# Performance work log

Measured on AMD Instinct MI355X. Metric: run time of the kernel, lower is better.

Reference implementation:

```python
import jax, jax.numpy as jnp
import numpy as np
from jax.ops import segment_sum

N = 50000        # nodes
E = 800000       # edges (avg degree 16)
H = 128          # hidden_dim
N_ITER = 2       # BCRefinement n_iterations
TIE_P = 0.05     # fraction of tie (boundary) edges


def setup_inputs() -> dict:
    key = jax.random.key(0)
    ks = jax.random.split(key, 24)
    s = 0.02
    inp = {
        'h': jax.random.normal(ks[0], (N, H), jnp.float32),
        'e': jax.random.normal(ks[1], (E, H), jnp.float32),
        'edge_attr_raw': jax.random.normal(ks[2], (E, 10), jnp.float32),
        # edge_refine: Linear(3H,2H) -> ReLU -> Linear(2H,H)
        'W_er1': s * jax.random.normal(ks[3], (3 * H, 2 * H), jnp.float32),
        'b_er1': jnp.zeros((2 * H,), jnp.float32),
        'W_er2': s * jax.random.normal(ks[4], (2 * H, H), jnp.float32),
        'b_er2': jnp.zeros((H,), jnp.float32),
        # GRUCell(H,H) torch layout: [3H, H] chunks (r, z, n)
        'W_ih': s * jax.random.normal(ks[5], (3 * H, H), jnp.float32),
        'W_hh': s * jax.random.normal(ks[6], (3 * H, H), jnp.float32),
        'b_ih': jnp.zeros((3 * H,), jnp.float32),
        'b_hh': jnp.zeros((3 * H,), jnp.float32),
        # node_neigh_fc: Linear(H,H)
        'W_nn': s * jax.random.normal(ks[7], (H, H), jnp.float32),
        'b_nn': jnp.zeros((H,), jnp.float32),
        # gate_mlp: Linear(3H,H) -> ReLU -> Linear(H,1), last bias init -2.0
        'W_g1': s * jax.random.normal(ks[8], (3 * H, H), jnp.float32),
        'b_g1': jnp.zeros((H,), jnp.float32),
        'W_g2': s * jax.random.normal(ks[9], (H, 1), jnp.float32),
        'b_g2': jnp.full((1,), -2.0, jnp.float32),
        'edge_index': jax.random.randint(ks[10], (2, E), 0, N, jnp.int32),
        'is_tie': jax.random.uniform(ks[11], (E,)) < TIE_P,
    }
    return inp


def reference(h, e, edge_attr_raw,
              W_er1, b_er1, W_er2, b_er2,
              W_ih, W_hh, b_ih, b_hh,
              W_nn, b_nn,
              W_g1, b_g1, W_g2, b_g2,
              edge_index, is_tie):
    row = edge_index[0]
    col = edge_index[1]
    tie_f = is_tie.astype(h.dtype)                        # [E]
    internal = ~is_tie

    # coupling buses: endpoints of any tie edge (tie-incidence count > 0)
    cpl_cnt = segment_sum(tie_f, row, num_segments=N) + \
              segment_sum(tie_f, col, num_segments=N)     # [N]
    is_cpl = cpl_cnt > 0

    # internal edges pointing into coupling buses; b_smooth weights w = 1/sqrt(X^2+eps)
    to_cpl = internal & is_cpl[col]
    X = jnp.abs(edge_attr_raw[:, 1])
    w = jnp.where(to_cpl, 1.0 / jnp.sqrt(X * X + 1e-6), 0.0)
    w_den = segment_sum(w, col, num_segments=N)           # [N]
    w_norm = w / (w_den[col] + 1e-6)                      # [E], zero off-mask

    deg = jnp.maximum(cpl_cnt, 1.0)                       # clamp_min(1.0)

    h_work, e_work = h, e
    for _ in range(N_ITER):
        # --- tie-edge refinement (applied only on tie edges) ---
        edge_in = jnp.concatenate([e_work, h_work[row], h_work[col]], axis=-1)  # [E,3H]
        e_ref = jax.nn.relu(edge_in @ W_er1 + b_er1) @ W_er2 + b_er2            # [E,H]
        e_work = e_work + tie_f[:, None] * e_ref

        # --- node messages from internal neighbors into coupling buses ---
        m_node_msg = h_work[row] @ W_nn + b_nn                                   # [E,H]
        m_node_all = segment_sum(m_node_msg * w_norm[:, None], col,
                                 num_segments=N)                                 # [N,H]

        # --- mean of incident tie-edge features at each node ---
        tie_e = tie_f[:, None] * e_work                                          # [E,H]
        m_edge_all = (segment_sum(tie_e, row, num_segments=N) +
                      segment_sum(tie_e, col, num_segments=N)) / deg[:, None]    # [N,H]

        # --- gating + GRU update on coupling buses ---
        gate_in = jnp.concatenate([m_edge_all, m_node_all, h_work], axis=-1)     # [N,3H]
        gate = jax.nn.sigmoid(jax.nn.relu(gate_in @ W_g1 + b_g1) @ W_g2 + b_g2)  # [N,1]
        m = m_edge_all + gate * m_node_all                                       # [N,H]

        gi = m @ W_ih.T + b_ih                                                   # [N,3H]
        gh = h_work @ W_hh.T + b_hh
        r = jax.nn.sigmoid(gi[:, :H] + gh[:, :H])
        z = jax.nn.sigmoid(gi[:, H:2 * H] + gh[:, H:2 * H])
        n = jnp.tanh(gi[:, 2 * H:] + r * gh[:, 2 * H:])
        h_new = (1.0 - z) * n + z * h_work

        h_work = jnp.where(is_cpl[:, None], h_new, h_work)
    return h_work, e_work
```

## Files before the change

kernel.cpp:

```cpp
#include <hip/hip_runtime.h>
#include <cstdint>

#define N_NODES 50000
#define N_EDGES 800000
#define HDIM    128
#define TIE_CAP 44000
#define NITER   2
#define SCAN_B  256

typedef __attribute__((ext_vector_type(8))) short bf16x8;
typedef __attribute__((ext_vector_type(4))) float f32x4;

__device__ __forceinline__ uint32_t f2bf(float f) {
    uint32_t u = __builtin_bit_cast(uint32_t, f);
    return (u + 0x7fffu + ((u >> 16) & 1u)) >> 16;
}
__device__ __forceinline__ float bf2f(uint32_t b) {
    return __builtin_bit_cast(float, b << 16);
}
__device__ __forceinline__ uint32_t comb2(uint32_t me, uint32_t mn, float g) {
    float a0 = bf2f(me & 0xffffu) + g * bf2f(mn & 0xffffu);
    float a1 = bf2f(me >> 16)     + g * bf2f(mn >> 16);
    return f2bf(a0) | (f2bf(a1) << 16);
}


__device__ __forceinline__ void stage_a128(const float* __restrict__ base,
                                           const int* __restrict__ gidx,
                                           int m0, int Mlim, char* tile, int tid)
{
    const int c = tid & 15;
    #pragma unroll
    for (int p = 0; p < 4; ++p) {
        int row = p * 32 + (tid >> 4);
        int ar = m0 + row; if (ar >= Mlim) ar = Mlim - 1;
        long g = gidx ? gidx[ar] : ar;
        const float* s = base + g * HDIM + c * 4;
        float4 v0 = *(const float4*)s;
        float4 v1 = *(const float4*)(s + 64);
        uint2 w0 = make_uint2(f2bf(v0.x) | (f2bf(v0.y) << 16),
                              f2bf(v0.z) | (f2bf(v0.w) << 16));
        uint2 w1 = make_uint2(f2bf(v1.x) | (f2bf(v1.y) << 16),
                              f2bf(v1.z) | (f2bf(v1.w) << 16));
        int sw = (row & 7) << 4;
        *(uint2*)(tile + row * 256 + ((c * 8) ^ sw)) = w0;
        *(uint2*)(tile + row * 256 + ((c * 8 + 128) ^ sw)) = w1;
    }
}

__device__ __forceinline__ void stage_bf128(const uint16_t* __restrict__ base,
                                            const int* __restrict__ gidx,
                                            int m0, int Mlim, char* tile, int tid)
{
    const int c = tid & 15;
    #pragma unroll
    for (int p = 0; p < 4; ++p) {
        int row = p * 32 + (tid >> 4);
        int ar = m0 + row; if (ar >= Mlim) ar = Mlim - 1;
        long g = gidx ? gidx[ar] : ar;
        uint4 v = *(const uint4*)(base + g * HDIM + c * 8);
        *(uint4*)(tile + row * 256 + ((c * 16) ^ ((row & 7) << 4))) = v;
    }
}

__device__ __forceinline__ void stage_b128(const short* __restrict__ BT, int ldk,
                                           int n0, int k0, char* tile, int tid)
{
    const int c = tid & 15;
    #pragma unroll
    for (int p = 0; p < 4; ++p) {
        int n = p * 32 + (tid >> 4);
        uint4 v = *(const uint4*)&BT[(size_t)(n0 + n) * ldk + k0 + c * 8];
        *(uint4*)(tile + n * 256 + ((c * 16) ^ ((n & 7) << 4))) = v;
    }
}

__device__ __forceinline__ void mfma128(const char* At, const char* Bt,
                                        int wr, int wc, int lane, f32x4 acc[4][2])
{
    #pragma unroll
    for (int ks = 0; ks < 4; ++ks) {
        int kb = ks * 64 + (lane >> 4) * 16;
        bf16x8 aF[4], bF[2];
        #pragma unroll
        for (int mi = 0; mi < 4; ++mi) {
            int row = wr * 64 + mi * 16 + (lane & 15);
            aF[mi] = *(const bf16x8*)(At + row * 256 + (kb ^ ((row & 7) << 4)));
        }
        #pragma unroll
        for (int ni = 0; ni < 2; ++ni) {
            int n = wc * 32 + ni * 16 + (lane & 15);
            bF[ni] = *(const bf16x8*)(Bt + n * 256 + (kb ^ ((n & 7) << 4)));
        }
        #pragma unroll
        for (int mi = 0; mi < 4; ++mi)
            #pragma unroll
            for (int ni = 0; ni < 2; ++ni)
                acc[mi][ni] = __builtin_amdgcn_mfma_f32_16x16x32_bf16(
                    aF[mi], bF[ni], acc[mi][ni], 0, 0, 0);
    }
}

__global__ __launch_bounds__(512)
void k_tie_fused(float* __restrict__ out_e, const uint16_t* __restrict__ h_bf,
                 const int* __restrict__ tie_cnt_p,
                 const int* __restrict__ tie_list, const int* __restrict__ tie_row,
                 const int* __restrict__ tie_col,
                 const short* __restrict__ BTer1, const short* __restrict__ BTer2,
                 const float* __restrict__ b_er1, const float* __restrict__ b_er2,
                 const float* __restrict__ deg_inv, float* __restrict__ m_edge)
{
    int cnt = *tie_cnt_p; if (cnt > TIE_CAP) cnt = TIE_CAP;
    const int m0 = blockIdx.x * 128;
    if (m0 >= cnt) return;

    __shared__ __align__(16) char At[32 * 1024];
    __shared__ __align__(16) char B0[32 * 1024];
    __shared__ __align__(16) char B1[32 * 1024];

    const int tid = threadIdx.x, lane = tid & 63;
    const int wid = tid >> 6, wr = wid >> 2, wc = wid & 3;

    f32x4 acc0[4][2] = {}, acc1[4][2] = {};
    #pragma unroll 1
    for (int c = 0; c < 3; ++c) {
        if (c == 0) stage_a128(out_e, tie_list, m0, cnt, At, tid);
        else        stage_bf128(h_bf, (c == 1) ? tie_row : tie_col, m0, cnt, At, tid);
        stage_b128(BTer1, 384, 0,   c * 128, B0, tid);
        stage_b128(BTer1, 384, 128, c * 128, B1, tid);
        __syncthreads();
        mfma128(At, B0, wr, wc, lane, acc0);
        mfma128(At, B1, wr, wc, lane, acc1);
        __syncthreads();
    }

    #pragma unroll
    for (int half = 0; half < 2; ++half) {
        char* Ct = half ? B0 : At;
        #pragma unroll
        for (int ni = 0; ni < 2; ++ni) {
            int col = wc * 32 + ni * 16 + (lane & 15);
            float bv = b_er1[half * 128 + col];
            #pragma unroll
            for (int mi = 0; mi < 4; ++mi)
                #pragma unroll
                for (int j = 0; j < 4; ++j) {
                    int rl = wr * 64 + mi * 16 + ((lane >> 4) << 2) + j;
                    float v = fmaxf((half ? acc1 : acc0)[mi][ni][j] + bv, 0.f);
                    *(uint16_t*)(Ct + rl * 256 + ((col * 2) ^ ((rl & 7) << 4))) =
                        (uint16_t)f2bf(v);
                }
        }
    }
    stage_b128(BTer2, 256, 0, 0, B1, tid);
    __syncthreads();
    f32x4 acc2[4][2] = {};
    mfma128(At, B1, wr, wc, lane, acc2);
    __syncthreads();
    stage_b128(BTer2, 256, 0, 128, B1, tid);
    __syncthreads();
    mfma128(B0, B1, wr, wc, lane, acc2);

    int col0 = wc * 32 + (lane & 15);
    float bv0 = b_er2[col0], bv1 = b_er2[col0 + 16];
    #pragma unroll
    for (int mi = 0; mi < 4; ++mi) {
        #pragma unroll
        for (int j = 0; j < 4; ++j) {
            int i = m0 + wr * 64 + mi * 16 + ((lane >> 4) << 2) + j;
            if (i < cnt) {
                int e = tie_list[i], r = tie_row[i], cc = tie_col[i];
                float dr = deg_inv[r], dc = deg_inv[cc];
                #pragma unroll
                for (int ni = 0; ni < 2; ++ni) {
                    int col = col0 + ni * 16;
                    float er = acc2[mi][ni][j] + (ni ? bv1 : bv0);
                    size_t eb = (size_t)e * HDIM + col;
                    float v = out_e[eb] + er;
                    out_e[eb] = v;
                    atomicAdd(&m_edge[(size_t)r * HDIM + col], v * dr);
                    atomicAdd(&m_edge[(size_t)cc * HDIM + col], v * dc);
                }
            }
        }
    }
}

__global__ __launch_bounds__(512)
void k_node_mega(const float* __restrict__ m_edge, const uint16_t* __restrict__ agg,
                 float* __restrict__ out_h, uint16_t* __restrict__ h_bf,
                 const float* __restrict__ cpl_cnt, const float* __restrict__ sumw,
                 const short* __restrict__ BTnn, const float* __restrict__ b_nn,
                 const short* __restrict__ BTg1, const float* __restrict__ b_g1,
                 const float* __restrict__ Wg2, const float* __restrict__ b_g2,
                 const short* __restrict__ BTcomb,
                 const short* __restrict__ BTihn, const short* __restrict__ BThhn,
                 const float* __restrict__ b_ih, const float* __restrict__ b_hh)
{
    const int m0 = blockIdx.x * 128;
    __shared__ __align__(16) char Tme[32 * 1024];
    __shared__ __align__(16) char Tmn[32 * 1024];
    __shared__ __align__(16) char Th [32 * 1024];
    __shared__ __align__(16) char Bt [32 * 1024];
    __shared__ float g_red[4][128];
    __shared__ float g_fin[128];
    __shared__ float sw_s[128];

    const int tid = threadIdx.x, lane = tid & 63;
    const int wid = tid >> 6, wr = wid >> 2, wc = wid & 3;

    stage_a128(m_edge, nullptr, m0, N_NODES, Tme, tid);
    stage_bf128(agg,   nullptr, m0, N_NODES, Tmn, tid);
    stage_bf128(h_bf,  nullptr, m0, N_NODES, Th,  tid);
    stage_b128(BTnn, 128, 0, 0, Bt, tid);
    if (tid < 128) {
        int n = m0 + tid; if (n >= N_NODES) n = N_NODES - 1;
        sw_s[tid] = sumw[n];
    }
    __syncthreads();

    {
        f32x4 accM[4][2] = {};
        mfma128(Tmn, Bt, wr, wc, lane, accM);
        __syncthreads();
        #pragma unroll
        for (int ni = 0; ni < 2; ++ni) {
            int col = wc * 32 + ni * 16 + (lane & 15);
            float bv = b_nn[col];
            #pragma unroll
            for (int mi = 0; mi < 4; ++mi)
                #pragma unroll
                for (int j = 0; j < 4; ++j) {
                    int rl = wr * 64 + mi * 16 + ((lane >> 4) << 2) + j;
                    float v = accM[mi][ni][j] + sw_s[rl] * bv;
                    *(uint16_t*)(Tmn + rl * 256 + ((col * 2) ^ ((rl & 7) << 4))) =
                        (uint16_t)f2bf(v);
                }
        }
        __syncthreads();
    }

    f32x4 accG[4][2] = {};
    #pragma unroll 1
    for (int c = 0; c < 3; ++c) {
        const char* Ac = (c == 0) ? Tme : (c == 1) ? Tmn : Th;
        stage_b128(BTg1, 384, 0, c * 128, Bt, tid);
        __syncthreads();
        mfma128(Ac, Bt, wr, wc, lane, accG);
        __syncthreads();
    }
    {
        float bg[2], wg[2];
        #pragma unroll
        for (int ni = 0; ni < 2; ++ni) {
            int col = wc * 32 + ni * 16 + (lane & 15);
            bg[ni] = b_g1[col]; wg[ni] = Wg2[col];
        }
        #pragma unroll
        for (int mi = 0; mi < 4; ++mi)
            #pragma unroll
            for (int j = 0; j < 4; ++j) {
                float p = fmaxf(accG[mi][0][j] + bg[0], 0.f) * wg[0]
                        + fmaxf(accG[mi][1][j] + bg[1], 0.f) * wg[1];
                #pragma unroll
                for (int o = 8; o; o >>= 1) p += __shfl_xor(p, o);
                if ((lane & 15) == 0)
                    g_red[wc][wr * 64 + mi * 16 + ((lane >> 4) << 2) + j] = p;
            }
    }
    __syncthreads();
    if (tid < 128) {
        float t = g_red[0][tid] + g_red[1][tid] + g_red[2][tid] + g_red[3][tid]
                + b_g2[0];
        g_fin[tid] = 1.f / (1.f + __expf(-t));
    }
    __syncthreads();

    {
        const int c = tid & 15;
        #pragma unroll
        for (int p = 0; p < 4; ++p) {
            int row = p * 32 + (tid >> 4);
            float g = g_fin[row];
            int sw = (row & 7) << 4;
            #pragma unroll
            for (int hh = 0; hh < 2; ++hh) {
                int off = (c * 8 + hh * 128) ^ sw;
                uint2 me2 = *(uint2*)(Tme + row * 256 + off);
                uint2 mn2 = *(uint2*)(Tmn + row * 256 + off);
                uint2 o2 = make_uint2(comb2(me2.x, mn2.x, g), comb2(me2.y, mn2.y, g));
                *(uint2*)(Tmn + row * 256 + off) = o2;
            }
        }
    }
    __syncthreads();

    f32x4 aR[4][2] = {}, aZ[4][2] = {}, aGI[4][2] = {}, aGH[4][2] = {};
    stage_b128(BTcomb, 256, 0, 0, Bt, tid);   __syncthreads();
    mfma128(Tmn, Bt, wr, wc, lane, aR);       __syncthreads();
    stage_b128(BTcomb, 256, 0, 128, Bt, tid); __syncthreads();
    mfma128(Th, Bt, wr, wc, lane, aR);        __syncthreads();
    stage_b128(BTcomb, 256, 128, 0, Bt, tid); __syncthreads();
    mfma128(Tmn, Bt, wr, wc, lane, aZ);       __syncthreads();
    stage_b128(BTcomb, 256, 128, 128, Bt, tid); __syncthreads();
    mfma128(Th, Bt, wr, wc, lane, aZ);        __syncthreads();
    stage_b128(BTihn, 128, 0, 0, Bt, tid);    __syncthreads();
    mfma128(Tmn, Bt, wr, wc, lane, aGI);      __syncthreads();
    stage_b128(BThhn, 128, 0, 0, Bt, tid);    __syncthreads();
    mfma128(Th, Bt, wr, wc, lane, aGH);

    #pragma unroll
    for (int ni = 0; ni < 2; ++ni) {
        int col = wc * 32 + ni * 16 + (lane & 15);
        float br  = b_ih[col] + b_hh[col];
        float bz  = b_ih[128 + col] + b_hh[128 + col];
        float bin = b_ih[256 + col], bhn = b_hh[256 + col];
        #pragma unroll
        for (int mi = 0; mi < 4; ++mi)
            #pragma unroll
            for (int j = 0; j < 4; ++j) {
                int node = m0 + wr * 64 + mi * 16 + ((lane >> 4) << 2) + j;
                if (node < N_NODES && cpl_cnt[node] > 0.f) {
                    float r = 1.f / (1.f + __expf(-(aR[mi][ni][j] + br)));
                    float z = 1.f / (1.f + __expf(-(aZ[mi][ni][j] + bz)));
                    float nn = tanhf(aGI[mi][ni][j] + bin + r * (aGH[mi][ni][j] + bhn));
                    size_t hb = (size_t)node * HDIM + col;
                    float hv = out_h[hb];
                    float hn = (1.f - z) * nn + z * hv;
                    out_h[hb] = hn;
                    h_bf[hb] = (uint16_t)f2bf(hn);
                }
            }
    }
}

__global__ __launch_bounds__(256)
void k_mnode_gather(const int* __restrict__ row_ptr, const int* __restrict__ csr_row,
                    const float* __restrict__ csr_w, const uint16_t* __restrict__ h_bf,
                    uint16_t* __restrict__ agg)
{
    int n = blockIdx.x * 4 + (threadIdx.x >> 6);
    if (n >= N_NODES) return;
    int lane = threadIdx.x & 63;
    int s = row_ptr[n], t = row_ptr[n + 1];
    float a0 = 0.f, a1 = 0.f;
    for (int j = s; j < t; ++j) {
        int r = csr_row[j];
        float w = csr_w[j];
        uint32_t v = *(const uint32_t*)(h_bf + (size_t)r * HDIM + lane * 2);
        a0 += w * bf2f(v & 0xffffu);
        a1 += w * bf2f(v >> 16);
    }
    *(uint32_t*)(agg + (size_t)n * HDIM + lane * 2) = f2bf(a0) | (f2bf(a1) << 16);
}

__global__ __launch_bounds__(256)
void k_prepw(const float* __restrict__ W, short* __restrict__ BT,
             int Kd, int Nd, int trans, int total)
{
    int i = blockIdx.x * 256 + threadIdx.x;
    if (i >= total) return;
    int n = i / Kd, k = i % Kd;
    float v = trans ? W[(size_t)k * Nd + n] : W[i];
    BT[i] = (short)f2bf(v);
}

__global__ __launch_bounds__(256)
void k_prepcomb(const float* __restrict__ W_ih, const float* __restrict__ W_hh,
                short* __restrict__ BTcomb)
{
    int i = blockIdx.x * 256 + threadIdx.x;
    if (i >= 256 * 256) return;
    int n = i >> 8, k = i & 255;
    float v = (k < 128) ? W_ih[n * 128 + k] : W_hh[n * 128 + (k - 128)];
    BTcomb[i] = (short)f2bf(v);
}

__global__ __launch_bounds__(256)
void k_h2bf(const float* __restrict__ h, uint16_t* __restrict__ h_bf)
{
    int i = blockIdx.x * 256 + threadIdx.x;
    if (i >= N_NODES * HDIM / 2) return;
    float2 v = *(const float2*)(h + (size_t)i * 2);
    *(uint32_t*)(h_bf + (size_t)i * 2) = f2bf(v.x) | (f2bf(v.y) << 16);
}

__global__ void k_detect(const uint8_t* __restrict__ tie_raw, int* __restrict__ fmt)
{
    __shared__ int cnt;
    if (threadIdx.x == 0) cnt = 0;
    __syncthreads();
    int c = 0;
    for (int i = threadIdx.x; i < 4096; i += 256)
        if ((i & 3) != 0 && tie_raw[i]) c++;
    if (c) atomicAdd(&cnt, c);
    __syncthreads();
    if (threadIdx.x == 0) *fmt = (cnt > 0) ? 1 : 0;
}

__device__ __forceinline__ bool is_tie_e(const void* raw, int fmt, int e)
{
    return fmt ? (((const uint8_t*)raw)[e] != 0) : (((const int*)raw)[e] != 0);
}

__global__ __launch_bounds__(256)
void k_tie(const void* __restrict__ tie_raw, const int* __restrict__ fmt_p,
           const int* __restrict__ ei, float* __restrict__ cpl_cnt,
           int* __restrict__ tie_cnt, int* __restrict__ tie_list,
           int* __restrict__ tie_row, int* __restrict__ tie_col)
{
    int e = blockIdx.x * 256 + threadIdx.x;
    if (e >= N_EDGES) return;
    if (!is_tie_e(tie_raw, *fmt_p, e)) return;
    int r = ei[e], c = ei[N_EDGES + e];
    atomicAdd(&cpl_cnt[r], 1.f);
    atomicAdd(&cpl_cnt[c], 1.f);
    int idx = atomicAdd(tie_cnt, 1);
    if (idx < TIE_CAP) { tie_list[idx] = e; tie_row[idx] = r; tie_col[idx] = c; }
}

__global__ __launch_bounds__(256)
void k_w(const void* __restrict__ tie_raw, const int* __restrict__ fmt_p,
         const int* __restrict__ ei, const float* __restrict__ attr,
         const float* __restrict__ cpl_cnt, float* __restrict__ w_den,
         float* __restrict__ w_arr, int* __restrict__ hist)
{
    int e = blockIdx.x * 256 + threadIdx.x;
    if (e >= N_EDGES) return;
    float w = 0.f;
    if (!is_tie_e(tie_raw, *fmt_p, e)) {
        int c = ei[N_EDGES + e];
        if (cpl_cnt[c] > 0.f) {
            float X = fabsf(attr[(size_t)e * 10 + 1]);
            w = 1.f / sqrtf(X * X + 1e-6f);
            atomicAdd(&w_den[c], w);
            atomicAdd(&hist[c], 1);
        }
    }
    w_arr[e] = w;
}

__global__ __launch_bounds__(256)
void k_wnorm(const int* __restrict__ ei, const float* __restrict__ w_den,
             float* __restrict__ w_arr)
{
    int e = blockIdx.x * 256 + threadIdx.x;
    if (e >= N_EDGES) return;
    float w = w_arr[e];
    if (w != 0.f) {
        int c = ei[N_EDGES + e];
        w_arr[e] = w / (w_den[c] + 1e-6f);
    }
}

__global__ __launch_bounds__(256)
void k_deg(const float* __restrict__ cpl_cnt, const float* __restrict__ w_den,
           float* __restrict__ deg_inv, float* __restrict__ sumw)
{
    int n = blockIdx.x * 256 + threadIdx.x;
    if (n >= N_NODES) return;
    deg_inv[n] = 1.f / fmaxf(cpl_cnt[n], 1.f);
    float wd = w_den[n];
    sumw[n] = wd / (wd + 1e-6f);
}

__global__ __launch_bounds__(SCAN_B)
void k_scan1(const int* __restrict__ cnt, int* __restrict__ excl,
             int* __restrict__ bsum, int n)
{
    __shared__ int s[SCAN_B];
    int t = threadIdx.x;
    int i = blockIdx.x * SCAN_B + t;
    int v = (i < n) ? cnt[i] : 0;
    s[t] = v;
    __syncthreads();
    for (int o = 1; o < SCAN_B; o <<= 1) {
        int u = (t >= o) ? s[t - o] : 0;
        __syncthreads();
        s[t] += u;
        __syncthreads();
    }
    if (i < n) excl[i] = s[t] - v;
    if (t == SCAN_B - 1) bsum[blockIdx.x] = s[t];
}

__global__ void k_scan2(int* __restrict__ bsum, int nb, int* __restrict__ total)
{
    if (threadIdx.x == 0) {
        int run = 0;
        for (int b = 0; b < nb; ++b) { int x = bsum[b]; bsum[b] = run; run += x; }
        *total = run;
    }
}

__global__ __launch_bounds__(256)
void k_scan3(const int* __restrict__ excl, const int* __restrict__ bsum,
             int* __restrict__ row_ptr, int* __restrict__ cursor,
             const int* __restrict__ total, int n)
{
    int i = blockIdx.x * 256 + threadIdx.x;
    if (i < n) {
        int v = excl[i] + bsum[i >> 8];
        row_ptr[i] = v;
        cursor[i] = v;
    }
    if (i == n) row_ptr[n] = *total;
}

__global__ __launch_bounds__(256)
void k_fill(const int* __restrict__ ei, const float* __restrict__ w_arr,
            int* __restrict__ cursor, int* __restrict__ csr_row,
            float* __restrict__ csr_w)
{
    int e = blockIdx.x * 256 + threadIdx.x;
    if (e >= N_EDGES) return;
    float w = w_arr[e];
    if (w == 0.f) return;
    int c = ei[N_EDGES + e];
    int pos = atomicAdd(&cursor[c], 1);
    csr_row[pos] = ei[e];
    csr_w[pos] = w;
}

extern "C" void kernel_launch(void* const* d_in, const int* in_sizes, int n_in,
                              void* d_out, int out_size, void* d_ws, size_t ws_size,
                              hipStream_t stream)
{
    const float* h     = (const float*)d_in[0];
    const float* e     = (const float*)d_in[1];
    const float* attr  = (const float*)d_in[2];
    const float* W_er1 = (const float*)d_in[3];
    const float* b_er1 = (const float*)d_in[4];
    const float* W_er2 = (const float*)d_in[5];
    const float* b_er2 = (const float*)d_in[6];
    const float* W_ih  = (const float*)d_in[7];
    const float* W_hh  = (const float*)d_in[8];
    const float* b_ih  = (const float*)d_in[9];
    const float* b_hh  = (const float*)d_in[10];
    const float* W_nn  = (const float*)d_in[11];
    const float* b_nn  = (const float*)d_in[12];
    const float* W_g1  = (const float*)d_in[13];
    const float* b_g1  = (const float*)d_in[14];
    const float* W_g2  = (const float*)d_in[15];
    const float* b_g2  = (const float*)d_in[16];
    const int*   ei    = (const int*)d_in[17];
    const void*  tie_raw = d_in[18];

    float* out_h = (float*)d_out;
    float* out_e = out_h + (size_t)N_NODES * HDIM;

    char* ws = (char*)d_ws;
    size_t off = 0;
    auto alloc = [&](size_t bytes) -> void* {
        void* p = ws + off;
        off = (off + bytes + 255) & ~(size_t)255;
        return p;
    };
    float* cpl_cnt = (float*)alloc((size_t)N_NODES * 4);
    float* w_den   = (float*)alloc((size_t)N_NODES * 4);
    int*   hist    = (int*)  alloc((size_t)N_NODES * 4);
    int*   counters= (int*)  alloc(256);
    size_t zero_bytes = off;
    float* deg_inv = (float*)alloc((size_t)N_NODES * 4);
    float* sumw    = (float*)alloc((size_t)N_NODES * 4);
    float* w_arr   = (float*)alloc((size_t)N_EDGES * 4);
    int* tie_list  = (int*)alloc((size_t)TIE_CAP * 4);
    int* tie_row   = (int*)alloc((size_t)TIE_CAP * 4);
    int* tie_col   = (int*)alloc((size_t)TIE_CAP * 4);
    short* BTer1   = (short*)alloc((size_t)256 * 384 * 2);
    short* BTer2   = (short*)alloc((size_t)128 * 256 * 2);
    short* BTnn    = (short*)alloc((size_t)128 * 128 * 2);
    short* BTg1    = (short*)alloc((size_t)128 * 384 * 2);
    short* BTcomb  = (short*)alloc((size_t)256 * 256 * 2);
    short* BTihn   = (short*)alloc((size_t)128 * 128 * 2);
    short* BThhn   = (short*)alloc((size_t)128 * 128 * 2);
    uint16_t* h_bf = (uint16_t*)alloc((size_t)N_NODES * HDIM * 2);
    uint16_t* agg  = (uint16_t*)alloc((size_t)N_NODES * HDIM * 2);
    float* m_edge  = (float*)alloc((size_t)N_NODES * HDIM * 4);
    int* excl      = (int*)alloc((size_t)N_NODES * 4);
    int* bsum      = (int*)alloc(256 * 4);
    int* row_ptr   = (int*)alloc((size_t)(N_NODES + 1) * 4);
    int* cursor    = (int*)alloc((size_t)N_NODES * 4);
    int* csr_row   = (int*)alloc((size_t)N_EDGES * 4);
    float* csr_w   = (float*)alloc((size_t)N_EDGES * 4);
    if (off > ws_size) return;

    int* fmt_p     = counters;
    int* tie_cnt   = counters + 1;
    int* csr_total = counters + 2;

    const int EB   = N_EDGES / 256;
    const int GM_T = (TIE_CAP + 127) / 128;
    const int GM_N = (N_NODES + 127) / 128;
    const int NB   = (N_NODES + SCAN_B - 1) / SCAN_B;

    hipMemsetAsync(d_ws, 0, zero_bytes, stream);
    k_detect<<<1, 256, 0, stream>>>((const uint8_t*)tie_raw, fmt_p);
    hipMemcpyAsync(out_h, h, (size_t)N_NODES * HDIM * 4, hipMemcpyDeviceToDevice, stream);
    hipMemcpyAsync(out_e, e, (size_t)N_EDGES * HDIM * 4, hipMemcpyDeviceToDevice, stream);
    k_h2bf<<<(N_NODES * HDIM / 2 + 255) / 256, 256, 0, stream>>>(h, h_bf);

    k_prepw<<<(384*256+255)/256, 256, 0, stream>>>(W_er1, BTer1, 384, 256, 1, 384*256);
    k_prepw<<<(256*128+255)/256, 256, 0, stream>>>(W_er2, BTer2, 256, 128, 1, 256*128);
    k_prepw<<<(128*128+255)/256, 256, 0, stream>>>(W_nn,  BTnn,  128, 128, 1, 128*128);
    k_prepw<<<(384*128+255)/256, 256, 0, stream>>>(W_g1,  BTg1,  384, 128, 1, 384*128);
    k_prepcomb<<<(256*256+255)/256, 256, 0, stream>>>(W_ih, W_hh, BTcomb);
    k_prepw<<<(128*128+255)/256, 256, 0, stream>>>(W_ih + 256*128, BTihn, 128, 128, 0, 128*128);
    k_prepw<<<(128*128+255)/256, 256, 0, stream>>>(W_hh + 256*128, BThhn, 128, 128, 0, 128*128);

    k_tie<<<EB, 256, 0, stream>>>(tie_raw, fmt_p, ei, cpl_cnt, tie_cnt, tie_list, tie_row, tie_col);
    k_w<<<EB, 256, 0, stream>>>(tie_raw, fmt_p, ei, attr, cpl_cnt, w_den, w_arr, hist);
    k_wnorm<<<EB, 256, 0, stream>>>(ei, w_den, w_arr);
    k_deg<<<(N_NODES + 255) / 256, 256, 0, stream>>>(cpl_cnt, w_den, deg_inv, sumw);

    k_scan1<<<NB, SCAN_B, 0, stream>>>(hist, excl, bsum, N_NODES);
    k_scan2<<<1, 64, 0, stream>>>(bsum, NB, csr_total);
    k_scan3<<<(N_NODES + 256) / 256, 256, 0, stream>>>(excl, bsum, row_ptr, cursor, csr_total, N_NODES);
    k_fill<<<EB, 256, 0, stream>>>(ei, w_arr, cursor, csr_row, csr_w);

    for (int it = 0; it < NITER; ++it) {
        hipMemsetAsync(m_edge, 0, (size_t)N_NODES * HDIM * 4, stream);
        k_tie_fused<<<GM_T, 512, 0, stream>>>(
            out_e, h_bf, tie_cnt, tie_list, tie_row, tie_col,
            BTer1, BTer2, b_er1, b_er2, deg_inv, m_edge);
        k_mnode_gather<<<(N_NODES + 3) / 4, 256, 0, stream>>>(row_ptr, csr_row, csr_w, h_bf, agg);
        k_node_mega<<<GM_N, 512, 0, stream>>>(
            m_edge, agg, out_h, h_bf, cpl_cnt, sumw,
            BTnn, b_nn, BTg1, b_g1, W_g2, b_g2,
            BTcomb, BTihn, BThhn, b_ih, b_hh);
    }
}
```

Before: 949.4 us.

## Consolidate setup kernels and move per-iteration m_edge zeroing into node kernel

Merges the many small setup launches (memset, detect, h copy/convert, seven weight-prep kernels, wnorm, deg) into fewer kernels. Tie compaction now takes one atomic per wavefront using ballot/popcount. Edge-weight normalisation moves into k_fill, and degree/sumw into k_scan3. m_edge is now zeroed by k_node_mega after it has been staged into LDS, which removes the per-iteration memset, at the cost of extra global stores in the node kernel and some restructuring risk.

```diff
diff --git a/kernel.cpp b/kernel.cpp
--- a/kernel.cpp
+++ b/kernel.cpp
@@ -79,7 +79,28 @@
                                         int wr, int wc, int lane, f32x4 acc[4][2])
 {
     #pragma unroll
-    for (int ks = 0; ks < 4; ++ks) {
+    for (int ks = 0; ks < 2; ++ks) {
+        int kb = ks * 64 + (lane >> 4) * 16;
+        bf16x8 aF[4], bF[2];
+        #pragma unroll
+        for (int mi = 0; mi < 4; ++mi) {
+            int row = wr * 64 + mi * 16 + (lane & 15);
+            aF[mi] = *(const bf16x8*)(At + row * 256 + (kb ^ ((row & 7) << 4)));
+        }
+        #pragma unroll
+        for (int ni = 0; ni < 2; ++ni) {
+            int n = wc * 32 + ni * 16 + (lane & 15);
+            bF[ni] = *(const bf16x8*)(Bt + n * 256 + (kb ^ ((n & 7) << 4)));
+        }
+        #pragma unroll
+        for (int mi = 0; mi < 4; ++mi)
+            #pragma unroll
+            for (int ni = 0; ni < 2; ++ni)
+                acc[mi][ni] = __builtin_amdgcn_mfma_f32_16x16x32_bf16(
+                    aF[mi], bF[ni], acc[mi][ni], 0, 0, 0);
+    }
+    #pragma unroll
+    for (int ks = 2; ks < 4; ++ks) {
         int kb = ks * 64 + (lane >> 4) * 16;
         bf16x8 aF[4], bF[2];
         #pragma unroll
@@ -187,7 +208,7 @@
 }
 
 __global__ __launch_bounds__(512)
-void k_node_mega(const float* __restrict__ m_edge, const uint16_t* __restrict__ agg,
+void k_node_mega(float* __restrict__ m_edge, const uint16_t* __restrict__ agg,
                  float* __restrict__ out_h, uint16_t* __restrict__ h_bf,
                  const float* __restrict__ cpl_cnt, const float* __restrict__ sumw,
                  const short* __restrict__ BTnn, const float* __restrict__ b_nn,
@@ -218,6 +239,13 @@
         sw_s[tid] = sumw[n];
     }
     __syncthreads();
+
+    {
+        int lim = (N_NODES - m0 < 128 ? N_NODES - m0 : 128) * HDIM / 4;
+        float4* mp = (float4*)(m_edge + (size_t)m0 * HDIM);
+        for (int i2 = tid; i2 < lim; i2 += 512)
+            mp[i2] = make_float4(0.f, 0.f, 0.f, 0.f);
+    }
 
     {
         f32x4 accM[4][2] = {};
@@ -288,8 +316,8 @@
                 int off = (c * 8 + hh * 128) ^ sw;
                 uint2 me2 = *(uint2*)(Tme + row * 256 + off);
                 uint2 mn2 = *(uint2*)(Tmn + row * 256 + off);
-                uint2 o2 = make_uint2(comb2(me2.x, mn2.x, g), comb2(me2.y, mn2.y, g));
-                *(uint2*)(Tmn + row * 256 + off) = o2;
+                *(uint2*)(Tmn + row * 256 + off) =
+                    make_uint2(comb2(me2.x, mn2.x, g), comb2(me2.y, mn2.y, g));
             }
         }
     }
@@ -355,80 +383,119 @@
 }
 
 __global__ __launch_bounds__(256)
-void k_prepw(const float* __restrict__ W, short* __restrict__ BT,
-             int Kd, int Nd, int trans, int total)
+void k_zero(float* cpl_cnt, float* w_den, int* hist, int* counters,
+            float* m_edge, const uint8_t* tie_raw)
+{
+    int gtid = blockIdx.x * 256 + threadIdx.x;
+    int gstr = gridDim.x * 256;
+    for (int i = gtid; i < N_NODES; i += gstr) {
+        cpl_cnt[i] = 0.f; w_den[i] = 0.f; hist[i] = 0;
+    }
+    for (int i = gtid; i < N_NODES * HDIM / 4; i += gstr)
+        ((float4*)m_edge)[i] = make_float4(0.f, 0.f, 0.f, 0.f);
+    if (blockIdx.x == 0 && threadIdx.x < 64) {
+        int c = 0;
+        for (int k = threadIdx.x; k < 4096; k += 64)
+            if ((k & 3) && tie_raw[k]) c = 1;
+        unsigned long long m = __ballot(c != 0);
+        if (threadIdx.x == 0) {
+            counters[0] = (m != 0ull) ? 1 : 0;
+            counters[1] = 0; counters[2] = 0;
+        }
+    }
+}
+
+__global__ __launch_bounds__(256)
+void k_hprep(const float* __restrict__ h, float* __restrict__ out_h,
+             uint16_t* __restrict__ h_bf)
+{
+    int gtid = blockIdx.x * 256 + threadIdx.x;
+    int gstr = gridDim.x * 256;
+    for (int i = gtid; i < N_NODES * HDIM / 4; i += gstr) {
+        float4 v = ((const float4*)h)[i];
+        ((float4*)out_h)[i] = v;
+        *(uint2*)(h_bf + (size_t)i * 4) =
+            make_uint2(f2bf(v.x) | (f2bf(v.y) << 16), f2bf(v.z) | (f2bf(v.w) << 16));
+    }
+}
+
+__global__ __launch_bounds__(256)
+void k_prepw_all(const float* W_er1, const float* W_er2, const float* W_nn,
+                 const float* W_g1, const float* W_ih, const float* W_hh,
+                 short* BTer1, short* BTer2, short* BTnn, short* BTg1,
+                 short* BTcomb, short* BTihn, short* BThhn)
 {
     int i = blockIdx.x * 256 + threadIdx.x;
-    if (i >= total) return;
-    int n = i / Kd, k = i % Kd;
-    float v = trans ? W[(size_t)k * Nd + n] : W[i];
-    BT[i] = (short)f2bf(v);
-}
-
-__global__ __launch_bounds__(256)
-void k_prepcomb(const float* __restrict__ W_ih, const float* __restrict__ W_hh,
-                short* __restrict__ BTcomb)
-{
-    int i = blockIdx.x * 256 + threadIdx.x;
-    if (i >= 256 * 256) return;
-    int n = i >> 8, k = i & 255;
-    float v = (k < 128) ? W_ih[n * 128 + k] : W_hh[n * 128 + (k - 128)];
-    BTcomb[i] = (short)f2bf(v);
-}
-
-__global__ __launch_bounds__(256)
-void k_h2bf(const float* __restrict__ h, uint16_t* __restrict__ h_bf)
-{
-    int i = blockIdx.x * 256 + threadIdx.x;
-    if (i >= N_NODES * HDIM / 2) return;
-    float2 v = *(const float2*)(h + (size_t)i * 2);
-    *(uint32_t*)(h_bf + (size_t)i * 2) = f2bf(v.x) | (f2bf(v.y) << 16);
-}
-
-__global__ void k_detect(const uint8_t* __restrict__ tie_raw, int* __restrict__ fmt)
-{
-    __shared__ int cnt;
-    if (threadIdx.x == 0) cnt = 0;
-    __syncthreads();
-    int c = 0;
-    for (int i = threadIdx.x; i < 4096; i += 256)
-        if ((i & 3) != 0 && tie_raw[i]) c++;
-    if (c) atomicAdd(&cnt, c);
-    __syncthreads();
-    if (threadIdx.x == 0) *fmt = (cnt > 0) ? 1 : 0;
-}
-
-__device__ __forceinline__ bool is_tie_e(const void* raw, int fmt, int e)
-{
-    return fmt ? (((const uint8_t*)raw)[e] != 0) : (((const int*)raw)[e] != 0);
-}
-
-__global__ __launch_bounds__(256)
-void k_tie(const void* __restrict__ tie_raw, const int* __restrict__ fmt_p,
+    if (i < 384 * 256) {
+        int n = i / 384, k = i % 384;
+        BTer1[i] = (short)f2bf(W_er1[(size_t)k * 256 + n]);
+    }
+    if (i < 128 * 256) {
+        int n = i / 256, k = i % 256;
+        BTer2[i] = (short)f2bf(W_er2[(size_t)k * 128 + n]);
+    }
+    if (i < 128 * 128) {
+        int n = i / 128, k = i % 128;
+        BTnn[i] = (short)f2bf(W_nn[(size_t)k * 128 + n]);
+    }
+    if (i < 128 * 384) {
+        int n = i / 384, k = i % 384;
+        BTg1[i] = (short)f2bf(W_g1[(size_t)k * 128 + n]);
+    }
+    if (i < 256 * 256) {
+        int n = i >> 8, k = i & 255;
+        float v = (k < 128) ? W_ih[n * 128 + k] : W_hh[n * 128 + (k - 128)];
+        BTcomb[i] = (short)f2bf(v);
+    }
+    if (i < 128 * 128) {
+        BTihn[i] = (short)f2bf(W_ih[256 * 128 + i]);
+        BThhn[i] = (short)f2bf(W_hh[256 * 128 + i]);
+    }
+}
+
+__global__ __launch_bounds__(256)
+void k_tie(const void* __restrict__ tie_raw, const int* __restrict__ counters,
            const int* __restrict__ ei, float* __restrict__ cpl_cnt,
            int* __restrict__ tie_cnt, int* __restrict__ tie_list,
            int* __restrict__ tie_row, int* __restrict__ tie_col)
 {
     int e = blockIdx.x * 256 + threadIdx.x;
-    if (e >= N_EDGES) return;
-    if (!is_tie_e(tie_raw, *fmt_p, e)) return;
-    int r = ei[e], c = ei[N_EDGES + e];
-    atomicAdd(&cpl_cnt[r], 1.f);
-    atomicAdd(&cpl_cnt[c], 1.f);
-    int idx = atomicAdd(tie_cnt, 1);
-    if (idx < TIE_CAP) { tie_list[idx] = e; tie_row[idx] = r; tie_col[idx] = c; }
-}
-
-__global__ __launch_bounds__(256)
-void k_w(const void* __restrict__ tie_raw, const int* __restrict__ fmt_p,
+    int fmt = counters[0];
+    bool t = false; int r = 0, c = 0;
+    if (e < N_EDGES)
+        t = fmt ? (((const uint8_t*)tie_raw)[e] != 0)
+                : (((const int*)tie_raw)[e] != 0);
+    if (t) {
+        r = ei[e]; c = ei[N_EDGES + e];
+        atomicAdd(&cpl_cnt[r], 1.f);
+        atomicAdd(&cpl_cnt[c], 1.f);
+    }
+    unsigned long long m = __ballot(t);
+    if (m == 0ull) return;
+    int lane = threadIdx.x & 63;
+    int first = __ffsll((unsigned long long)m) - 1;
+    int base = 0;
+    if (lane == first) base = atomicAdd(tie_cnt, __popcll(m));
+    base = __shfl(base, first);
+    if (t) {
+        int idx = base + __popcll(m & ((1ull << lane) - 1ull));
+        if (idx < TIE_CAP) { tie_list[idx] = e; tie_row[idx] = r; tie_col[idx] = c; }
+    }
+}
+
+__global__ __launch_bounds__(256)
+void k_w(const void* __restrict__ tie_raw, const int* __restrict__ counters,
          const int* __restrict__ ei, const float* __restrict__ attr,
          const float* __restrict__ cpl_cnt, float* __restrict__ w_den,
          float* __restrict__ w_arr, int* __restrict__ hist)
 {
     int e = blockIdx.x * 256 + threadIdx.x;
     if (e >= N_EDGES) return;
+    int fmt = counters[0];
+    bool t = fmt ? (((const uint8_t*)tie_raw)[e] != 0)
+                 : (((const int*)tie_raw)[e] != 0);
     float w = 0.f;
-    if (!is_tie_e(tie_raw, *fmt_p, e)) {
+    if (!t) {
         int c = ei[N_EDGES + e];
         if (cpl_cnt[c] > 0.f) {
             float X = fabsf(attr[(size_t)e * 10 + 1]);
@@ -440,38 +507,14 @@
     w_arr[e] = w;
 }
 
-__global__ __launch_bounds__(256)
-void k_wnorm(const int* __restrict__ ei, const float* __restrict__ w_den,
-             float* __restrict__ w_arr)
-{
-    int e = blockIdx.x * 256 + threadIdx.x;
-    if (e >= N_EDGES) return;
-    float w = w_arr[e];
-    if (w != 0.f) {
-        int c = ei[N_EDGES + e];
-        w_arr[e] = w / (w_den[c] + 1e-6f);
-    }
-}
-
-__global__ __launch_bounds__(256)
-void k_deg(const float* __restrict__ cpl_cnt, const float* __restrict__ w_den,
-           float* __restrict__ deg_inv, float* __restrict__ sumw)
-{
-    int n = blockIdx.x * 256 + threadIdx.x;
-    if (n >= N_NODES) return;
-    deg_inv[n] = 1.f / fmaxf(cpl_cnt[n], 1.f);
-    float wd = w_den[n];
-    sumw[n] = wd / (wd + 1e-6f);
-}
-
 __global__ __launch_bounds__(SCAN_B)
-void k_scan1(const int* __restrict__ cnt, int* __restrict__ excl,
-             int* __restrict__ bsum, int n)
+void k_scan1(const int* __restrict__ hist, int* __restrict__ excl,
+             int* __restrict__ bsum)
 {
     __shared__ int s[SCAN_B];
     int t = threadIdx.x;
     int i = blockIdx.x * SCAN_B + t;
-    int v = (i < n) ? cnt[i] : 0;
+    int v = (i < N_NODES) ? hist[i] : 0;
     s[t] = v;
     __syncthreads();
     for (int o = 1; o < SCAN_B; o <<= 1) {
@@ -480,37 +523,43 @@
         s[t] += u;
         __syncthreads();
     }
-    if (i < n) excl[i] = s[t] - v;
+    if (i < N_NODES) excl[i] = s[t] - v;
     if (t == SCAN_B - 1) bsum[blockIdx.x] = s[t];
 }
 
-__global__ void k_scan2(int* __restrict__ bsum, int nb, int* __restrict__ total)
-{
+__global__ void k_scan2(int* __restrict__ bsum, int* __restrict__ counters)
+{
+    const int NB = (N_NODES + SCAN_B - 1) / SCAN_B;
     if (threadIdx.x == 0) {
         int run = 0;
-        for (int b = 0; b < nb; ++b) { int x = bsum[b]; bsum[b] = run; run += x; }
-        *total = run;
+        for (int b = 0; b < NB; ++b) { int x = bsum[b]; bsum[b] = run; run += x; }
+        counters[2] = run;
     }
 }
 
 __global__ __launch_bounds__(256)
 void k_scan3(const int* __restrict__ excl, const int* __restrict__ bsum,
              int* __restrict__ row_ptr, int* __restrict__ cursor,
-             const int* __restrict__ total, int n)
+             const int* __restrict__ counters,
+             const float* __restrict__ cpl_cnt, const float* __restrict__ w_den,
+             float* __restrict__ deg_inv, float* __restrict__ sumw)
 {
     int i = blockIdx.x * 256 + threadIdx.x;
-    if (i < n) {
+    if (i < N_NODES) {
         int v = excl[i] + bsum[i >> 8];
         row_ptr[i] = v;
         cursor[i] = v;
-    }
-    if (i == n) row_ptr[n] = *total;
+        deg_inv[i] = 1.f / fmaxf(cpl_cnt[i], 1.f);
+        float wd = w_den[i];
+        sumw[i] = wd / (wd + 1e-6f);
+    }
+    if (i == N_NODES) row_ptr[N_NODES] = counters[2];
 }
 
 __global__ __launch_bounds__(256)
 void k_fill(const int* __restrict__ ei, const float* __restrict__ w_arr,
-            int* __restrict__ cursor, int* __restrict__ csr_row,
-            float* __restrict__ csr_w)
+            const float* __restrict__ w_den, int* __restrict__ cursor,
+            int* __restrict__ csr_row, float* __restrict__ csr_w)
 {
     int e = blockIdx.x * 256 + threadIdx.x;
     if (e >= N_EDGES) return;
@@ -519,7 +568,7 @@
     int c = ei[N_EDGES + e];
     int pos = atomicAdd(&cursor[c], 1);
     csr_row[pos] = ei[e];
-    csr_w[pos] = w;
+    csr_w[pos] = w / (w_den[c] + 1e-6f);
 }
 
 extern "C" void kernel_launch(void* const* d_in, const int* in_sizes, int n_in,
@@ -560,7 +609,6 @@
     float* w_den   = (float*)alloc((size_t)N_NODES * 4);
     int*   hist    = (int*)  alloc((size_t)N_NODES * 4);
     int*   counters= (int*)  alloc(256);
-    size_t zero_bytes = off;
     float* deg_inv = (float*)alloc((size_t)N_NODES * 4);
     float* sumw    = (float*)alloc((size_t)N_NODES * 4);
     float* w_arr   = (float*)alloc((size_t)N_EDGES * 4);
@@ -585,45 +633,37 @@
     float* csr_w   = (float*)alloc((size_t)N_EDGES * 4);
     if (off > ws_size) return;
 
-    int* fmt_p     = counters;
-    int* tie_cnt   = counters + 1;
-    int* csr_total = counters + 2;
+    int* tie_cnt = counters + 1;
 
     const int EB   = N_EDGES / 256;
     const int GM_T = (TIE_CAP + 127) / 128;
     const int GM_N = (N_NODES + 127) / 128;
     const int NB   = (N_NODES + SCAN_B - 1) / SCAN_B;
 
-    hipMemsetAsync(d_ws, 0, zero_bytes, stream);
-    k_detect<<<1, 256, 0, stream>>>((const uint8_t*)tie_raw, fmt_p);
-    hipMemcpyAsync(out_h, h, (size_t)N_NODES * HDIM * 4, hipMemcpyDeviceToDevice, stream);
-    hipMemcpyAsync(out_e, e, (size_t)N_EDGES * HDIM * 4, hipMemcpyDeviceToDevice, stream);
-    k_h2bf<<<(N_NODES * HDIM / 2 + 255) / 256, 256, 0, stream>>>(h, h_bf);
-
-    k_prepw<<<(384*256+255)/256, 256, 0, stream>>>(W_er1, BTer1, 384, 256, 1, 384*256);
-    k_prepw<<<(256*128+255)/256, 256, 0, stream>>>(W_er2, BTer2, 256, 128, 1, 256*128);
-    k_prepw<<<(128*128+255)/256, 256, 0, stream>>>(W_nn,  BTnn,  128, 128, 1, 128*128);
-    k_prepw<<<(384*128+255)/256, 256, 0, stream>>>(W_g1,  BTg1,  384, 128, 1, 384*128);
-    k_prepcomb<<<(256*256+255)/256, 256, 0, stream>>>(W_ih, W_hh, BTcomb);
-    k_prepw<<<(128*128+255)/256, 256, 0, stream>>>(W_ih + 256*128, BTihn, 128, 128, 0, 128*128);
-    k_prepw<<<(128*128+255)/256, 256, 0, stream>>>(W_hh + 256*128, BThhn, 128, 128, 0, 128*128);
-
-    k_tie<<<EB, 256, 0, stream>>>(tie_raw, fmt_p, ei, cpl_cnt, tie_cnt, tie_list, tie_row, tie_col);
-    k_w<<<EB, 256, 0, stream>>>(tie_raw, fmt_p, ei, attr, cpl_cnt, w_den, w_arr, hist);
-    k_wnorm<<<EB, 256, 0, stream>>>(ei, w_den, w_arr);
-    k_deg<<<(N_NODES + 255) / 256, 256, 0, stream>>>(cpl_cnt, w_den, deg_inv, sumw);
-
-    k_scan1<<<NB, SCAN_B, 0, stream>>>(hist, excl, bsum, N_NODES);
-    k_scan2<<<1, 64, 0, stream>>>(bsum, NB, csr_total);
-    k_scan3<<<(N_NODES + 256) / 256, 256, 0, stream>>>(excl, bsum, row_ptr, cursor, csr_total, N_NODES);
-    k_fill<<<EB, 256, 0, stream>>>(ei, w_arr, cursor, csr_row, csr_w);
+    k_zero<<<400, 256, 0, stream>>>(cpl_cnt, w_den, hist, counters, m_edge,
+                                    (const uint8_t*)tie_raw);
+    hipMemcpyAsync(out_e, e, (size_t)N_EDGES * HDIM * 4,
+                   hipMemcpyDeviceToDevice, stream);
+    k_hprep<<<512, 256, 0, stream>>>(h, out_h, h_bf);
+    k_prepw_all<<<(384 * 256 + 255) / 256, 256, 0, stream>>>(
+        W_er1, W_er2, W_nn, W_g1, W_ih, W_hh,
+        BTer1, BTer2, BTnn, BTg1, BTcomb, BTihn, BThhn);
+    k_tie<<<EB, 256, 0, stream>>>(tie_raw, counters, ei, cpl_cnt,
+                                  tie_cnt, tie_list, tie_row, tie_col);
+    k_w<<<EB, 256, 0, stream>>>(tie_raw, counters, ei, attr, cpl_cnt,
+                                w_den, w_arr, hist);
+    k_scan1<<<NB, SCAN_B, 0, stream>>>(hist, excl, bsum);
+    k_scan2<<<1, 64, 0, stream>>>(bsum, counters);
+    k_scan3<<<(N_NODES + 256) / 256, 256, 0, stream>>>(
+        excl, bsum, row_ptr, cursor, counters, cpl_cnt, w_den, deg_inv, sumw);
+    k_fill<<<EB, 256, 0, stream>>>(ei, w_arr, w_den, cursor, csr_row, csr_w);
 
     for (int it = 0; it < NITER; ++it) {
-        hipMemsetAsync(m_edge, 0, (size_t)N_NODES * HDIM * 4, stream);
         k_tie_fused<<<GM_T, 512, 0, stream>>>(
             out_e, h_bf, tie_cnt, tie_list, tie_row, tie_col,
             BTer1, BTer2, b_er1, b_er2, deg_inv, m_edge);
-        k_mnode_gather<<<(N_NODES + 3) / 4, 256, 0, stream>>>(row_ptr, csr_row, csr_w, h_bf, agg);
+        k_mnode_gather<<<(N_NODES + 3) / 4, 256, 0, stream>>>(
+            row_ptr, csr_row, csr_w, h_bf, agg);
         k_node_mega<<<GM_N, 512, 0, stream>>>(
             m_edge, agg, out_h, h_bf, cpl_cnt, sumw,
             BTnn, b_nn, BTg1, b_g1, W_g2, b_g2,
```

Result: faster. 913.4 us (-3.8%).
